# Optimization experiments

Hardware: AMD Instinct MI355X
Metric: run time of the kernel (lower is better)

Reference implementation:

```python
import jax, jax.numpy as jnp
import numpy as np

B, F, L, P, H = 32, 64, 8192, 96, 8
HD = F // H
EPS_ATTN = 1e-6
EPS_REVIN = 1e-5
EPS_LN = 1e-5


def setup_inputs() -> dict:
    key = jax.random.key(0)
    ks = jax.random.split(key, 8)
    f32 = jnp.float32
    return {
        'x': jax.random.normal(ks[0], (B, F, L), dtype=f32),
        'gamma': jnp.ones((1, 1, F), dtype=f32),
        'beta': jnp.zeros((1, 1, F), dtype=f32),
        'ln_w': jnp.ones((F,), dtype=f32),
        'ln_b': jnp.zeros((F,), dtype=f32),
        'Wq': 0.05 * jax.random.normal(ks[1], (F, F), dtype=f32),
        'bq': jnp.zeros((F,), dtype=f32),
        'Wk': 0.05 * jax.random.normal(ks[2], (F, F), dtype=f32),
        'bk': jnp.zeros((F,), dtype=f32),
        'Wv': 0.05 * jax.random.normal(ks[3], (F, F), dtype=f32),
        'bv': jnp.zeros((F,), dtype=f32),
        'Wo': 0.05 * jax.random.normal(ks[4], (F, F), dtype=f32),
        'bo': jnp.zeros((F,), dtype=f32),
        'Wlin': 0.01 * jax.random.normal(ks[5], (P, L), dtype=f32),
        'blin': jnp.zeros((P,), dtype=f32),
        'Wp': 0.1 * jax.random.normal(ks[6], (1, F), dtype=f32),
        'bp': jnp.zeros((1,), dtype=f32),
    }


def _phi(t):
    # feature map: elu(x) + 1 (non-negative)
    return jax.nn.elu(t) + 1.0


def _layernorm(h, w, b):
    mu = jnp.mean(h, axis=-1, keepdims=True)
    var = jnp.mean(jnp.square(h - mu), axis=-1, keepdims=True)
    return (h - mu) * jax.lax.rsqrt(var + EPS_LN) * w + b


def reference(x, gamma, beta, ln_w, ln_b, Wq, bq, Wk, bk, Wv, bv, Wo, bo,
              Wlin, blin, Wp, bp):
    # (B, F, L) -> (B, L, F)
    xt = jnp.transpose(x, (0, 2, 1))
    # RevIN norm (stats over time axis, detached; torch std is unbiased ddof=1)
    mean = jax.lax.stop_gradient(jnp.mean(xt, axis=1, keepdims=True))
    std = jax.lax.stop_gradient(jnp.std(xt, axis=1, keepdims=True, ddof=1) + EPS_REVIN)
    xn = (xt - mean) / std * gamma + beta
    residual = xn
    h = _layernorm(xn, ln_w, ln_b)
    # Q/K/V projections (torch Linear: h @ W.T + b)
    Q = h @ Wq.T + bq
    K = h @ Wk.T + bk
    V = h @ Wv.T + bv
    # (B, L, F) -> (B, H, L, HD)
    def heads(t):
        return jnp.transpose(t.reshape(B, L, H, HD), (0, 2, 1, 3))
    Q, K, V = heads(Q), heads(K), heads(V)
    Q, K = _phi(Q), _phi(K)
    # linear attention: phi(Q) (phi(K)^T V) / (phi(Q) sum_n phi(K))
    KV = jnp.einsum('bhnd,bhne->bhde', K, V)           # (B,H,HD,HD)
    out = jnp.einsum('bhnd,bhde->bhne', Q, KV)          # (B,H,L,HD)
    Z = jnp.sum(K, axis=2)                              # (B,H,HD)
    normalizer = jnp.einsum('bhnd,bhd->bhn', Q, Z)[..., None] + EPS_ATTN
    out = out / normalizer
    out = jnp.transpose(out, (0, 2, 1, 3)).reshape(B, L, F)
    out = out @ Wo.T + bo
    y = out + residual                                  # (B, L, F)
    # temporal linear: (B, F, L) @ Wlin.T -> (B, F, P) -> (B, P, F)
    y = jnp.transpose(jnp.transpose(y, (0, 2, 1)) @ Wlin.T + blin, (0, 2, 1))
    # RevIN denorm
    y = (y - beta) / gamma
    y = y * std + mean
    # projector to scalar per step
    return (y @ Wp.T + bp)[..., 0]                      # (B, P)
```

## Files before the change

### kernel.cpp

```cpp
#include <hip/hip_runtime.h>
#include <cstddef>

#define NB 32
#define NF 64
#define NL 8192
#define NP 96
#define NH 8
#define TSPLIT 32

#define WS_MEAN 0
#define WS_STD  2048
#define WS_RSTD 4096
#define WS_KV   6144
#define WS_Z    22528
#define WS_OUT2 24576
#define WS_MUN  221184
#define WS_RSN  483328
#define WS_WLB  745472
#define WS_XNB  1138688
#define WS_YT   9527296

typedef __bf16 bfx8 __attribute__((ext_vector_type(8)));
typedef float f32x4 __attribute__((ext_vector_type(4)));
#define MFMA16(a, b, c) __builtin_amdgcn_mfma_f32_16x16x32_bf16((a), (b), (c), 0, 0, 0)

__device__ __forceinline__ unsigned short f2bf(float f) {
  unsigned u = __float_as_uint(f);
  unsigned r = u + 0x7FFFu + ((u >> 16) & 1u);
  return (unsigned short)(r >> 16);
}
__device__ __forceinline__ unsigned packbf2(float lo, float hi) {
  return (unsigned)f2bf(lo) | ((unsigned)f2bf(hi) << 16);
}
__device__ __forceinline__ float bflo(unsigned d) { return __uint_as_float(d << 16); }
__device__ __forceinline__ float bfhi(unsigned d) { return __uint_as_float(d & 0xFFFF0000u); }
__device__ __forceinline__ float bf1(unsigned short s) { return __uint_as_float(((unsigned)s) << 16); }

__device__ __forceinline__ bfx8 ldfrag(const unsigned short* p) {
  uint4 u = *(const uint4*)p;
  return __builtin_bit_cast(bfx8, u);
}

__global__ __launch_bounds__(256) void k_pre(
    const float* __restrict__ x, const float* __restrict__ Wlin,
    float* __restrict__ wmean, float* __restrict__ wstd, float* __restrict__ wrstd,
    unsigned short* __restrict__ wlb, float* __restrict__ zz) {
  __shared__ float r1[4], r2[4];
  const int bid = blockIdx.x, tid = threadIdx.x;
  if (bid < NB * NF) {
    const float4* row4 = (const float4*)(x + (size_t)bid * NL);
    float s1 = 0.f, s2 = 0.f;
#pragma unroll
    for (int i = 0; i < NL / 4 / 256; i++) {
      float4 v = row4[tid + i * 256];
      s1 += v.x + v.y + v.z + v.w;
      s2 += v.x * v.x + v.y * v.y + v.z * v.z + v.w * v.w;
    }
#pragma unroll
    for (int off = 32; off > 0; off >>= 1) {
      s1 += __shfl_down(s1, off, 64);
      s2 += __shfl_down(s2, off, 64);
    }
    if ((tid & 63) == 0) { r1[tid >> 6] = s1; r2[tid >> 6] = s2; }
    __syncthreads();
    if (tid == 0) {
      s1 = r1[0] + r1[1] + r1[2] + r1[3];
      s2 = r2[0] + r2[1] + r2[2] + r2[3];
      float m = s1 * (1.f / NL);
      float var = (s2 - (float)NL * m * m) * (1.f / (NL - 1));
      float sd = sqrtf(fmaxf(var, 0.f)) + 1e-5f;
      wmean[bid] = m;
      wstd[bid] = sd;
      wrstd[bid] = 1.f / sd;
    }
    unsigned zi = (unsigned)bid * 256u + (unsigned)tid;
    if (zi < 215040u) zz[zi] = 0.f;
  } else {
    int i = (bid - NB * NF) * 256 + tid;
    int p = i >> 10;
    int l8 = (i & 1023) * 8;
    float4 va = *(const float4*)&Wlin[(size_t)p * NL + l8];
    float4 vb = *(const float4*)&Wlin[(size_t)p * NL + l8 + 4];
    uint4 o;
    o.x = packbf2(va.x, va.y); o.y = packbf2(va.z, va.w);
    o.z = packbf2(vb.x, vb.y); o.w = packbf2(vb.z, vb.w);
    *(uint4*)&wlb[(((size_t)(l8 >> 5)) * NP + p) * 32 + (l8 & 31)] = o;
  }
}

__global__ __launch_bounds__(256, 4) void k_kv(
    const float* __restrict__ x,
    const float* __restrict__ gamma, const float* __restrict__ beta,
    const float* __restrict__ lnw, const float* __restrict__ lnb,
    const float* __restrict__ Wk, const float* __restrict__ bk,
    const float* __restrict__ Wv, const float* __restrict__ bv,
    const float* __restrict__ wmean, const float* __restrict__ wrstd,
    float* __restrict__ wKV, float* __restrict__ wZ,
    float* __restrict__ wmun, float* __restrict__ wrsn,
    unsigned short* __restrict__ xnb) {
  __shared__ __align__(16) char smem[39424];
  unsigned short* hA  = (unsigned short*)smem;
  unsigned short* WkB = (unsigned short*)(smem + 18432);
  unsigned short* WvB = (unsigned short*)(smem + 27648);
  unsigned short* pK  = (unsigned short*)smem;
  unsigned short* pV  = (unsigned short*)(smem + 17408);
  float* SkT  = (float*)(smem + 36864);
  float* mun  = (float*)(smem + 37888);
  float* rsn  = (float*)(smem + 38400);
  float* cbc  = (float*)(smem + 38912);

  const int tid = threadIdx.x;
  const int b = blockIdx.x >> 6;
  const int tI = blockIdx.x & 63;
  const int L0 = tI * 128;
  const int lane = tid & 63, wv = tid >> 6;
  const int mm = lane & 15, qd = lane >> 4;

  if (tid < 64) {
    float cb = wrstd[b * NF + tid] * gamma[tid];
    cbc[2 * tid] = cb;
    cbc[2 * tid + 1] = beta[tid] - wmean[b * NF + tid] * cb;
  }
  {
    int jj = tid >> 2, g = tid & 3;
    int f0 = g * 16;
    float tkp = 0.f, tvp = 0.f, skp = 0.f, svp = 0.f;
#pragma unroll
    for (int i = 0; i < 4; i++) {
      int f = f0 + i * 4;
      float4 wk4 = *(const float4*)&Wk[jj * NF + f];
      float4 wv4 = *(const float4*)&Wv[jj * NF + f];
      float4 lw  = *(const float4*)&lnw[f];
      float4 lb  = *(const float4*)&lnb[f];
      uint2 pk2, pv2;
      pk2.x = packbf2(wk4.x * lw.x, wk4.y * lw.y);
      pk2.y = packbf2(wk4.z * lw.z, wk4.w * lw.w);
      pv2.x = packbf2(wv4.x * lw.x, wv4.y * lw.y);
      pv2.y = packbf2(wv4.z * lw.z, wv4.w * lw.w);
      *(uint2*)&WkB[jj * 72 + f] = pk2;
      *(uint2*)&WvB[jj * 72 + f] = pv2;
      tkp += lb.x * wk4.x + lb.y * wk4.y + lb.z * wk4.z + lb.w * wk4.w;
      tvp += lb.x * wv4.x + lb.y * wv4.y + lb.z * wv4.z + lb.w * wv4.w;
      skp += bflo(pk2.x) + bfhi(pk2.x) + bflo(pk2.y) + bfhi(pk2.y);
      svp += bflo(pv2.x) + bfhi(pv2.x) + bflo(pv2.y) + bfhi(pv2.y);
    }
    tkp += __shfl_xor(tkp, 1, 64); tkp += __shfl_xor(tkp, 2, 64);
    tvp += __shfl_xor(tvp, 1, 64); tvp += __shfl_xor(tvp, 2, 64);
    skp += __shfl_xor(skp, 1, 64); skp += __shfl_xor(skp, 2, 64);
    svp += __shfl_xor(svp, 1, 64); svp += __shfl_xor(svp, 2, 64);
    if (g == 0) {
      SkT[jj]       = skp;
      SkT[64 + jj]  = tkp + bk[jj];
      SkT[128 + jj] = svp;
      SkT[192 + jj] = tvp + bv[jj];
    }
  }
  __syncthreads();

  {
    const int lt = tid >> 3;
    const int fg = tid & 7;
    const int l0q = lt * 4;
    const float* xp = x + ((size_t)(b * NF + fg * 8)) * NL + L0 + l0q;
    f32x4 v[8];
#pragma unroll
    for (int i = 0; i < 8; i++) v[i] = *(const f32x4*)(xp + (size_t)i * NL);
    float a[8][4];
#pragma unroll
    for (int i = 0; i < 4; i++) {
      float4 c = *(const float4*)&cbc[fg * 16 + i * 4];
#pragma unroll
      for (int j = 0; j < 4; j++) {
        a[2 * i][j]     = fmaf(v[2 * i][j], c.x, c.y);
        a[2 * i + 1][j] = fmaf(v[2 * i + 1][j], c.z, c.w);
      }
    }
    float s1[4], s2[4];
#pragma unroll
    for (int j = 0; j < 4; j++) {
      s1[j] = 0.f; s2[j] = 0.f;
#pragma unroll
      for (int i = 0; i < 8; i++) {
        s1[j] += a[i][j];
        s2[j] = fmaf(a[i][j], a[i][j], s2[j]);
      }
    }
#pragma unroll
    for (int m = 1; m <= 4; m <<= 1) {
#pragma unroll
      for (int j = 0; j < 4; j++) {
        s1[j] += __shfl_xor(s1[j], m, 64);
        s2[j] += __shfl_xor(s2[j], m, 64);
      }
    }
#pragma unroll
    for (int j = 0; j < 4; j++) {
      uint4 o;
      o.x = packbf2(a[0][j], a[1][j]);
      o.y = packbf2(a[2][j], a[3][j]);
      o.z = packbf2(a[4][j], a[5][j]);
      o.w = packbf2(a[6][j], a[7][j]);
      *(uint4*)&hA[(l0q + j) * 72 + fg * 8] = o;
      *(uint4*)(xnb + (((size_t)(b * 64 + tI) * 128 + l0q + j) * 64 + fg * 8)) = o;
    }
    if (fg == 0) {
      float mv[4], rv[4];
#pragma unroll
      for (int j = 0; j < 4; j++) {
        float mu = s1[j] * (1.f / NF);
        float var = s2[j] * (1.f / NF) - mu * mu;
        mv[j] = mu;
        rv[j] = rsqrtf(fmaxf(var, 0.f) + 1e-5f);
      }
      float4 m4 = {mv[0], mv[1], mv[2], mv[3]};
      float4 r4 = {rv[0], rv[1], rv[2], rv[3]};
      *(float4*)&mun[l0q] = m4;
      *(float4*)&rsn[l0q] = r4;
      *(float4*)&wmun[(size_t)b * NL + L0 + l0q] = m4;
      *(float4*)&wrsn[(size_t)b * NL + L0 + l0q] = r4;
    }
  }
  __syncthreads();

  const f32x4 fz = {0.f, 0.f, 0.f, 0.f};
  f32x4 kacc[2][4], vacc[2][4];
#pragma unroll
  for (int i = 0; i < 2; i++)
#pragma unroll
    for (int jt = 0; jt < 4; jt++) { kacc[i][jt] = fz; vacc[i][jt] = fz; }

#pragma unroll
  for (int kc = 0; kc < 2; kc++) {
    bfx8 a0 = ldfrag(&hA[(wv * 32 + mm) * 72 + kc * 32 + qd * 8]);
    bfx8 a1 = ldfrag(&hA[(wv * 32 + 16 + mm) * 72 + kc * 32 + qd * 8]);
#pragma unroll
    for (int jt = 0; jt < 4; jt++) {
      bfx8 bkf = ldfrag(&WkB[(jt * 16 + mm) * 72 + kc * 32 + qd * 8]);
      bfx8 bvf = ldfrag(&WvB[(jt * 16 + mm) * 72 + kc * 32 + qd * 8]);
      kacc[0][jt] = MFMA16(a0, bkf, kacc[0][jt]);
      kacc[1][jt] = MFMA16(a1, bkf, kacc[1][jt]);
      vacc[0][jt] = MFMA16(a0, bvf, vacc[0][jt]);
      vacc[1][jt] = MFMA16(a1, bvf, vacc[1][jt]);
    }
  }

#pragma unroll
  for (int lt2 = 0; lt2 < 2; lt2++) {
    float4 mu4 = *(const float4*)&mun[wv * 32 + lt2 * 16 + qd * 4];
    float4 rs4 = *(const float4*)&rsn[wv * 32 + lt2 * 16 + qd * 4];
    float muv[4] = {mu4.x, mu4.y, mu4.z, mu4.w};
    float rsv[4] = {rs4.x, rs4.y, rs4.z, rs4.w};
#pragma unroll
    for (int jt = 0; jt < 4; jt++) {
      int j = jt * 16 + mm;
      float Sk = SkT[j], Tk = SkT[64 + j], Sv = SkT[128 + j], Tv = SkT[192 + j];
#pragma unroll
      for (int r = 0; r < 4; r++) {
        float kk = rsv[r] * (kacc[lt2][jt][r] - muv[r] * Sk) + Tk;
        kacc[lt2][jt][r] = (kk > 0.f) ? (kk + 1.f) : __expf(kk);
        vacc[lt2][jt][r] = rsv[r] * (vacc[lt2][jt][r] - muv[r] * Sv) + Tv;
      }
    }
  }

  {
#pragma unroll
    for (int jt = 0; jt < 4; jt++) {
      float z = 0.f;
#pragma unroll
      for (int lt2 = 0; lt2 < 2; lt2++)
#pragma unroll
        for (int r = 0; r < 4; r++) z += kacc[lt2][jt][r];
      z += __shfl_xor(z, 16, 64);
      z += __shfl_xor(z, 32, 64);
      if (qd == 0) atomicAdd(&wZ[b * 64 + jt * 16 + mm], z);
    }
  }
  __syncthreads();

#pragma unroll
  for (int lt2 = 0; lt2 < 2; lt2++) {
    int l0 = wv * 32 + lt2 * 16 + qd * 4;
#pragma unroll
    for (int jt = 0; jt < 4; jt++) {
      int j = jt * 16 + mm;
      uint2 dk, dv;
      dk.x = packbf2(kacc[lt2][jt][0], kacc[lt2][jt][1]);
      dk.y = packbf2(kacc[lt2][jt][2], kacc[lt2][jt][3]);
      dv.x = packbf2(vacc[lt2][jt][0], vacc[lt2][jt][1]);
      dv.y = packbf2(vacc[lt2][jt][2], vacc[lt2][jt][3]);
      *(uint2*)&pK[j * 136 + l0] = dk;
      *(uint2*)&pV[j * 136 + l0] = dv;
    }
  }
  __syncthreads();

  {
    f32x4 racc = fz;
#pragma unroll
    for (int kb = 0; kb < 4; kb++) {
      bfx8 ak = ldfrag(&pK[(wv * 16 + mm) * 136 + kb * 32 + qd * 8]);
      bfx8 bv8 = ldfrag(&pV[(wv * 16 + mm) * 136 + kb * 32 + qd * 8]);
      racc = MFMA16(ak, bv8, racc);
    }
    int eh = mm >> 3, e = mm & 7;
#pragma unroll
    for (int r = 0; r < 4; r++) {
      int row = qd * 4 + r;
      if ((row >> 3) == eh)
        atomicAdd(&wKV[(b * NH + wv * 2 + eh) * 64 + (row & 7) * 8 + e], racc[r]);
    }
  }
}

__global__ __launch_bounds__(256, 4) void k_qy(
    const unsigned short* __restrict__ xnb,
    const float* __restrict__ lnw, const float* __restrict__ lnb,
    const float* __restrict__ Wq, const float* __restrict__ bq,
    const float* __restrict__ Wo, const float* __restrict__ bo,
    const float* __restrict__ wmun, const float* __restrict__ wrsn,
    const float* __restrict__ wKV, const float* __restrict__ wZ,
    unsigned short* __restrict__ ytb) {
  __shared__ __align__(16) char smem[40960];
  unsigned short* hA  = (unsigned short*)smem;
  unsigned short* qaA = (unsigned short*)smem;
  unsigned short* WqB = (unsigned short*)(smem + 18432);
  unsigned short* WoB = (unsigned short*)(smem + 27648);
  float* kvz   = (float*)(smem + 36864);
  float* mun   = (float*)(smem + 39424);
  float* rsn   = (float*)(smem + 39936);
  float* SqTq  = (float*)(smem + 40448);

  const int tid = threadIdx.x;
  const int b = blockIdx.x >> 6;
  const int tI = blockIdx.x & 63;
  const int L0 = tI * 128;
  const int lane = tid & 63, wv = tid >> 6;
  const int mm = lane & 15, qd = lane >> 4;
  const unsigned short* xtile = xnb + (size_t)(b * 64 + tI) * 128 * 64;

  {
    int jj = tid >> 2, g = tid & 3;
    int f0 = g * 16;
    float tqp = 0.f, sqp = 0.f;
#pragma unroll
    for (int i = 0; i < 4; i++) {
      int f = f0 + i * 4;
      float4 wq4 = *(const float4*)&Wq[jj * NF + f];
      float4 wo4 = *(const float4*)&Wo[jj * NF + f];
      float4 lw  = *(const float4*)&lnw[f];
      float4 lb  = *(const float4*)&lnb[f];
      uint2 pq2, po2;
      pq2.x = packbf2(wq4.x * lw.x, wq4.y * lw.y);
      pq2.y = packbf2(wq4.z * lw.z, wq4.w * lw.w);
      po2.x = packbf2(wo4.x, wo4.y);
      po2.y = packbf2(wo4.z, wo4.w);
      *(uint2*)&WqB[jj * 72 + f] = pq2;
      *(uint2*)&WoB[jj * 72 + f] = po2;
      tqp += lb.x * wq4.x + lb.y * wq4.y + lb.z * wq4.z + lb.w * wq4.w;
      sqp += bflo(pq2.x) + bfhi(pq2.x) + bflo(pq2.y) + bfhi(pq2.y);
    }
    tqp += __shfl_xor(tqp, 1, 64); tqp += __shfl_xor(tqp, 2, 64);
    sqp += __shfl_xor(sqp, 1, 64); sqp += __shfl_xor(sqp, 2, 64);
    if (g == 0) { SqTq[jj] = sqp; SqTq[64 + jj] = tqp + bq[jj]; }
  }
  for (int i = tid; i < 640; i += 256)
    kvz[i] = (i < 512) ? wKV[b * 512 + i] : (i < 576 ? wZ[b * 64 + i - 512] : bo[i - 576]);
  {
    int row = tid >> 1, half = tid & 1;
    const uint4* s4 = (const uint4*)(xtile + (size_t)row * 64 + half * 32);
    uint4 u0 = s4[0], u1 = s4[1], u2 = s4[2], u3 = s4[3];
    uint4* d4 = (uint4*)&hA[row * 72 + half * 32];
    d4[0] = u0; d4[1] = u1; d4[2] = u2; d4[3] = u3;
  }
  if (tid < 64) {
    int h = tid >> 5, i = tid & 31;
    const float* src = h ? wrsn : wmun;
    float4 v = *(const float4*)&src[(size_t)b * NL + L0 + i * 4];
    *(float4*)&((h ? rsn : mun)[i * 4]) = v;
  }
  __syncthreads();

  const f32x4 fz = {0.f, 0.f, 0.f, 0.f};
  f32x4 yacc[2][4];

  {
    f32x4 qacc[2][4];
#pragma unroll
    for (int i = 0; i < 2; i++)
#pragma unroll
      for (int jt = 0; jt < 4; jt++) qacc[i][jt] = fz;
#pragma unroll
    for (int kc = 0; kc < 2; kc++) {
      bfx8 a0 = ldfrag(&hA[(wv * 32 + mm) * 72 + kc * 32 + qd * 8]);
      bfx8 a1 = ldfrag(&hA[(wv * 32 + 16 + mm) * 72 + kc * 32 + qd * 8]);
#pragma unroll
      for (int jt = 0; jt < 4; jt++) {
        bfx8 bqf = ldfrag(&WqB[(jt * 16 + mm) * 72 + kc * 32 + qd * 8]);
        qacc[0][jt] = MFMA16(a0, bqf, qacc[0][jt]);
        qacc[1][jt] = MFMA16(a1, bqf, qacc[1][jt]);
      }
    }
#pragma unroll
    for (int lt2 = 0; lt2 < 2; lt2++) {
      int l0 = wv * 32 + lt2 * 16 + qd * 4;
#pragma unroll
      for (int ft = 0; ft < 4; ft++) {
        int ff = ft * 16 + mm;
        float bof = kvz[576 + ff];
#pragma unroll
        for (int r = 0; r < 4; r++)
          yacc[lt2][ft][r] = bf1(hA[(l0 + r) * 72 + ff]) + bof;
      }
    }
#pragma unroll
    for (int lt2 = 0; lt2 < 2; lt2++) {
      float4 mu4 = *(const float4*)&mun[wv * 32 + lt2 * 16 + qd * 4];
      float4 rs4 = *(const float4*)&rsn[wv * 32 + lt2 * 16 + qd * 4];
      float muv[4] = {mu4.x, mu4.y, mu4.z, mu4.w};
      float rsv[4] = {rs4.x, rs4.y, rs4.z, rs4.w};
      int l0 = wv * 32 + lt2 * 16 + qd * 4;
#pragma unroll
      for (int jt = 0; jt < 4; jt++) {
        int j = jt * 16 + mm;
        float Sj = SqTq[j], Tj = SqTq[64 + j];
#pragma unroll
        for (int r = 0; r < 4; r++) {
          float q = rsv[r] * (qacc[lt2][jt][r] - muv[r] * Sj) + Tj;
          q = (q > 0.f) ? (q + 1.f) : __expf(q);
          qaA[(l0 + r) * 72 + j] = f2bf(q);
        }
      }
    }
  }
  __syncthreads();

  {
    int lt = tid & 31, hd = tid >> 5;
    int lbase = lt * 4;
    float qv[4][8];
#pragma unroll
    for (int i = 0; i < 4; i++) {
      uint4 u = *(const uint4*)&qaA[(lbase + i) * 72 + hd * 8];
      qv[i][0] = bflo(u.x); qv[i][1] = bfhi(u.x);
      qv[i][2] = bflo(u.y); qv[i][3] = bfhi(u.y);
      qv[i][4] = bflo(u.z); qv[i][5] = bfhi(u.z);
      qv[i][6] = bflo(u.w); qv[i][7] = bfhi(u.w);
    }
    float att[4][8], nrm[4];
#pragma unroll
    for (int i = 0; i < 4; i++) {
      nrm[i] = 1e-6f;
#pragma unroll
      for (int e = 0; e < 8; e++) att[i][e] = 0.f;
    }
#pragma unroll
    for (int d = 0; d < 8; d++) {
      float zd = kvz[512 + hd * 8 + d];
      float4 kva = *(const float4*)&kvz[hd * 64 + d * 8];
      float4 kvb = *(const float4*)&kvz[hd * 64 + d * 8 + 4];
#pragma unroll
      for (int i = 0; i < 4; i++) {
        float qq = qv[i][d];
        nrm[i] = fmaf(qq, zd, nrm[i]);
        att[i][0] = fmaf(qq, kva.x, att[i][0]);
        att[i][1] = fmaf(qq, kva.y, att[i][1]);
        att[i][2] = fmaf(qq, kva.z, att[i][2]);
        att[i][3] = fmaf(qq, kva.w, att[i][3]);
        att[i][4] = fmaf(qq, kvb.x, att[i][4]);
        att[i][5] = fmaf(qq, kvb.y, att[i][5]);
        att[i][6] = fmaf(qq, kvb.z, att[i][6]);
        att[i][7] = fmaf(qq, kvb.w, att[i][7]);
      }
    }
#pragma unroll
    for (int i = 0; i < 4; i++) {
      float inv = 1.f / nrm[i];
      uint4 o;
      o.x = packbf2(att[i][0] * inv, att[i][1] * inv);
      o.y = packbf2(att[i][2] * inv, att[i][3] * inv);
      o.z = packbf2(att[i][4] * inv, att[i][5] * inv);
      o.w = packbf2(att[i][6] * inv, att[i][7] * inv);
      *(uint4*)&qaA[(lbase + i) * 72 + hd * 8] = o;
    }
  }
  __syncthreads();

  {
#pragma unroll
    for (int ec = 0; ec < 2; ec++) {
      bfx8 a0 = ldfrag(&qaA[(wv * 32 + mm) * 72 + ec * 32 + qd * 8]);
      bfx8 a1 = ldfrag(&qaA[(wv * 32 + 16 + mm) * 72 + ec * 32 + qd * 8]);
#pragma unroll
      for (int ft = 0; ft < 4; ft++) {
        bfx8 bof = ldfrag(&WoB[(ft * 16 + mm) * 72 + ec * 32 + qd * 8]);
        yacc[0][ft] = MFMA16(a0, bof, yacc[0][ft]);
        yacc[1][ft] = MFMA16(a1, bof, yacc[1][ft]);
      }
    }
#pragma unroll
    for (int lt2 = 0; lt2 < 2; lt2++) {
#pragma unroll
      for (int ft = 0; ft < 4; ft++) {
        int ff = ft * 16 + mm;
        uint2 o2;
        o2.x = packbf2(yacc[lt2][ft][0], yacc[lt2][ft][1]);
        o2.y = packbf2(yacc[lt2][ft][2], yacc[lt2][ft][3]);
        size_t idx = (((size_t)b * (NL / 32) + (L0 >> 5) + wv) * 64 + ff) * 32 + lt2 * 16 + qd * 4;
        *(uint2*)&ytb[idx] = o2;
      }
    }
  }
}

__global__ __launch_bounds__(256) void k_temporal(
    const unsigned short* __restrict__ ytb, const unsigned short* __restrict__ wlb,
    float* __restrict__ out2) {
  const int tid = threadIdx.x, lane = tid & 63, wvx = tid >> 6;
  const int mm = lane & 15, qd = lane >> 4;
  const int b = blockIdx.x / TSPLIT;
  const int kc = blockIdx.x % TSPLIT;
  const f32x4 fz = {0.f, 0.f, 0.f, 0.f};
  f32x4 acc[6];
#pragma unroll
  for (int pt = 0; pt < 6; pt++) acc[pt] = fz;

#pragma unroll 2
  for (int ks = 0; ks < 8; ks++) {
    int lg = kc * 8 + ks;
    bfx8 bfr = ldfrag(&ytb[(((size_t)b * (NL / 32) + lg) * 64 + wvx * 16 + mm) * 32 + qd * 8]);
#pragma unroll
    for (int pt = 0; pt < 6; pt++) {
      bfx8 afr = ldfrag(&wlb[((size_t)lg * NP + pt * 16 + mm) * 32 + qd * 8]);
      acc[pt] = MFMA16(afr, bfr, acc[pt]);
    }
  }
  const int ff = wvx * 16 + mm;
#pragma unroll
  for (int pt = 0; pt < 6; pt++) {
#pragma unroll
    for (int r = 0; r < 4; r++) {
      int p = pt * 16 + qd * 4 + r;
      atomicAdd(&out2[((size_t)(b * NP + p)) * NF + ff], acc[pt][r]);
    }
  }
}

__global__ __launch_bounds__(64) void k_final(
    const float* __restrict__ out2, const float* __restrict__ blin,
    const float* __restrict__ gamma, const float* __restrict__ beta,
    const float* __restrict__ wmean, const float* __restrict__ wstd,
    const float* __restrict__ Wp, const float* __restrict__ bp,
    float* __restrict__ out) {
  int b = blockIdx.x / NP;
  int p = blockIdx.x % NP;
  int f = threadIdx.x;
  float v = out2[((size_t)(b * NP + p)) * NF + f] + blin[p];
  v = (v - beta[f]) / gamma[f];
  v = v * wstd[b * NF + f] + wmean[b * NF + f];
  float s = v * Wp[f];
#pragma unroll
  for (int off = 32; off > 0; off >>= 1)
    s += __shfl_down(s, off, 64);
  if (f == 0) out[blockIdx.x] = s + bp[0];
}

extern "C" void kernel_launch(void* const* d_in, const int* in_sizes, int n_in,
                              void* d_out, int out_size, void* d_ws, size_t ws_size,
                              hipStream_t stream) {
  const float* x     = (const float*)d_in[0];
  const float* gamma = (const float*)d_in[1];
  const float* beta  = (const float*)d_in[2];
  const float* lnw   = (const float*)d_in[3];
  const float* lnb   = (const float*)d_in[4];
  const float* Wq    = (const float*)d_in[5];
  const float* bq    = (const float*)d_in[6];
  const float* Wk    = (const float*)d_in[7];
  const float* bk    = (const float*)d_in[8];
  const float* Wv    = (const float*)d_in[9];
  const float* bv    = (const float*)d_in[10];
  const float* Wo    = (const float*)d_in[11];
  const float* bo    = (const float*)d_in[12];
  const float* Wlin  = (const float*)d_in[13];
  const float* blin  = (const float*)d_in[14];
  const float* Wp    = (const float*)d_in[15];
  const float* bp    = (const float*)d_in[16];
  float* out = (float*)d_out;
  float* ws  = (float*)d_ws;

  float* wmean = ws + WS_MEAN;
  float* wstd  = ws + WS_STD;
  float* wrstd = ws + WS_RSTD;
  float* wKV   = ws + WS_KV;
  float* wZ    = ws + WS_Z;
  float* wout2 = ws + WS_OUT2;
  float* wmun  = ws + WS_MUN;
  float* wrsn  = ws + WS_RSN;
  unsigned short* wlb = (unsigned short*)(ws + WS_WLB);
  unsigned short* xnb = (unsigned short*)(ws + WS_XNB);
  unsigned short* ytb = (unsigned short*)(ws + WS_YT);

  k_pre<<<NB * NF + NP * NL / 8 / 256, 256, 0, stream>>>(x, Wlin, wmean, wstd, wrstd, wlb, wKV);
  k_kv<<<NB * 64, 256, 0, stream>>>(x, gamma, beta, lnw, lnb, Wk, bk, Wv, bv,
                                    wmean, wrstd, wKV, wZ, wmun, wrsn, xnb);
  k_qy<<<NB * 64, 256, 0, stream>>>(xnb, lnw, lnb, Wq, bq, Wo, bo,
                                    wmun, wrsn, wKV, wZ, ytb);
  k_temporal<<<NB * TSPLIT, 256, 0, stream>>>(ytb, wlb, wout2);
  k_final<<<NB * NP, 64, 0, stream>>>(wout2, blin, gamma, beta, wmean, wstd, Wp, bp, out);
}
```

Before: 230.5 us.

## Hoist global tile loads early, halve temporal split, batch final blocks

```diff
diff --git a/kernel.cpp b/kernel.cpp
--- a/kernel.cpp
+++ b/kernel.cpp
@@ -6,7 +6,7 @@
 #define NL 8192
 #define NP 96
 #define NH 8
-#define TSPLIT 32
+#define TSPLIT 16
 
 #define WS_MEAN 0
 #define WS_STD  2048
@@ -25,9 +25,8 @@
 #define MFMA16(a, b, c) __builtin_amdgcn_mfma_f32_16x16x32_bf16((a), (b), (c), 0, 0, 0)
 
 __device__ __forceinline__ unsigned short f2bf(float f) {
-  unsigned u = __float_as_uint(f);
-  unsigned r = u + 0x7FFFu + ((u >> 16) & 1u);
-  return (unsigned short)(r >> 16);
+  __bf16 h = (__bf16)f;
+  return __builtin_bit_cast(unsigned short, h);
 }
 __device__ __forceinline__ unsigned packbf2(float lo, float hi) {
   return (unsigned)f2bf(lo) | ((unsigned)f2bf(hi) << 16);
@@ -116,6 +115,14 @@
   const int lane = tid & 63, wv = tid >> 6;
   const int mm = lane & 15, qd = lane >> 4;
 
+  const int lt = tid >> 3;
+  const int fg = tid & 7;
+  const int l0q = lt * 4;
+  const float* xp = x + ((size_t)(b * NF + fg * 8)) * NL + L0 + l0q;
+  f32x4 v[8];
+#pragma unroll
+  for (int i = 0; i < 8; i++) v[i] = *(const f32x4*)(xp + (size_t)i * NL);
+
   if (tid < 64) {
     float cb = wrstd[b * NF + tid] * gamma[tid];
     cbc[2 * tid] = cb;
@@ -158,13 +165,6 @@
   __syncthreads();
 
   {
-    const int lt = tid >> 3;
-    const int fg = tid & 7;
-    const int l0q = lt * 4;
-    const float* xp = x + ((size_t)(b * NF + fg * 8)) * NL + L0 + l0q;
-    f32x4 v[8];
-#pragma unroll
-    for (int i = 0; i < 8; i++) v[i] = *(const f32x4*)(xp + (size_t)i * NL);
     float a[8][4];
 #pragma unroll
     for (int i = 0; i < 4; i++) {
@@ -339,6 +339,10 @@
   const int mm = lane & 15, qd = lane >> 4;
   const unsigned short* xtile = xnb + (size_t)(b * 64 + tI) * 128 * 64;
 
+  const int prow = tid >> 1, phalf = tid & 1;
+  const uint4* ps4 = (const uint4*)(xtile + (size_t)prow * 64 + phalf * 32);
+  uint4 pu0 = ps4[0], pu1 = ps4[1], pu2 = ps4[2], pu3 = ps4[3];
+
   {
     int jj = tid >> 2, g = tid & 3;
     int f0 = g * 16;
@@ -367,11 +371,8 @@
   for (int i = tid; i < 640; i += 256)
     kvz[i] = (i < 512) ? wKV[b * 512 + i] : (i < 576 ? wZ[b * 64 + i - 512] : bo[i - 576]);
   {
-    int row = tid >> 1, half = tid & 1;
-    const uint4* s4 = (const uint4*)(xtile + (size_t)row * 64 + half * 32);
-    uint4 u0 = s4[0], u1 = s4[1], u2 = s4[2], u3 = s4[3];
-    uint4* d4 = (uint4*)&hA[row * 72 + half * 32];
-    d4[0] = u0; d4[1] = u1; d4[2] = u2; d4[3] = u3;
+    uint4* d4 = (uint4*)&hA[prow * 72 + phalf * 32];
+    d4[0] = pu0; d4[1] = pu1; d4[2] = pu2; d4[3] = pu3;
   }
   if (tid < 64) {
     int h = tid >> 5, i = tid & 31;
@@ -526,8 +527,8 @@
   for (int pt = 0; pt < 6; pt++) acc[pt] = fz;
 
 #pragma unroll 2
-  for (int ks = 0; ks < 8; ks++) {
-    int lg = kc * 8 + ks;
+  for (int ks = 0; ks < NL / 32 / TSPLIT; ks++) {
+    int lg = kc * (NL / 32 / TSPLIT) + ks;
     bfx8 bfr = ldfrag(&ytb[(((size_t)b * (NL / 32) + lg) * 64 + wvx * 16 + mm) * 32 + qd * 8]);
 #pragma unroll
     for (int pt = 0; pt < 6; pt++) {
@@ -546,23 +547,23 @@
   }
 }
 
-__global__ __launch_bounds__(64) void k_final(
+__global__ __launch_bounds__(256) void k_final(
     const float* __restrict__ out2, const float* __restrict__ blin,
     const float* __restrict__ gamma, const float* __restrict__ beta,
     const float* __restrict__ wmean, const float* __restrict__ wstd,
-    const float* __restrict__ Wp, const float* __restrict__ bp,
+    const float* __restrict__ Wp, const float* __restrict__ bp0,
     float* __restrict__ out) {
-  int b = blockIdx.x / NP;
-  int p = blockIdx.x % NP;
-  int f = threadIdx.x;
-  float v = out2[((size_t)(b * NP + p)) * NF + f] + blin[p];
+  int bp = blockIdx.x * 4 + (threadIdx.x >> 6);
+  int f = threadIdx.x & 63;
+  int b = bp / NP, p = bp % NP;
+  float v = out2[(size_t)bp * NF + f] + blin[p];
   v = (v - beta[f]) / gamma[f];
   v = v * wstd[b * NF + f] + wmean[b * NF + f];
   float s = v * Wp[f];
 #pragma unroll
   for (int off = 32; off > 0; off >>= 1)
     s += __shfl_down(s, off, 64);
-  if (f == 0) out[blockIdx.x] = s + bp[0];
+  if (f == 0) out[bp] = s + bp0[0];
 }
 
 extern "C" void kernel_launch(void* const* d_in, const int* in_sizes, int n_in,
@@ -606,5 +607,5 @@
   k_qy<<<NB * 64, 256, 0, stream>>>(xnb, lnw, lnb, Wq, bq, Wo, bo,
                                     wmun, wrsn, wKV, wZ, ytb);
   k_temporal<<<NB * TSPLIT, 256, 0, stream>>>(ytb, wlb, wout2);
-  k_final<<<NB * NP, 64, 0, stream>>>(wout2, blin, gamma, beta, wmean, wstd, Wp, bp, out);
-}
+  k_final<<<NB * NP / 4, 256, 0, stream>>>(wout2, blin, gamma, beta, wmean, wstd, Wp, bp, out);
+}
```

After: 232.0 us. Within noise of the previous version (+0.7%).
